# Kernel optimization log

Measured on AMD Instinct MI355X. Metric: run time of the kernel, lower is better.

## Reference

```python
import jax, jax.numpy as jnp
import numpy as np

G = 5   # grid intervals
K = 5   # spline order
H = 2.0 / G  # knot spacing on [-1, 1]
# Extended uniform knot vector: G + 2K + 1 = 16 knots from -1-K*H to 1+K*H.
KNOTS = jnp.arange(-K, G + K + 1, dtype=jnp.float32) * H - 1.0  # (16,)


def bspline_bases(x):
    """Cox-de Boor B-spline bases. x: (B, in) -> (B, in, G+K)."""
    g = KNOTS[None, :]            # (1, 16), broadcasts over (B, in, .)
    xe = x[..., None]             # (B, in, 1)
    # degree-0 indicator bases: (B, in, G+2K)
    b = ((xe >= g[:, :-1]) & (xe < g[:, 1:])).astype(x.dtype)
    for d in range(1, K + 1):
        left = (xe - g[:, : -(d + 1)]) / (g[:, d:-1] - g[:, : -(d + 1)]) * b[..., :-1]
        right = (g[:, d + 1 :] - xe) / (g[:, d + 1 :] - g[:, 1:-d]) * b[..., 1:]
        b = left + right
    return b  # (B, in, G+K)


def kan_layer(x, Wb, Ws):
    # residual base path: silu(x) @ Wb  (in,out)
    # spline path: sum_i sum_k B[b,i,k] * Ws[i,o,k]
    bases = bspline_bases(x)
    return jax.nn.silu(x) @ Wb + jnp.einsum('bik,iok->bo', bases, Ws)


def setup_inputs() -> dict:
    key = jax.random.key(0)
    ks = jax.random.split(key, 7)
    B, IN, OUT, NB = 16384, 1024, 64, G + K
    s = 0.1  # small init scale
    return {
        'x':   jax.random.uniform(ks[0], (B, IN), dtype=jnp.float32),
        'Wb1': jax.random.normal(ks[1], (IN, 5), dtype=jnp.float32) * s,
        'Ws1': jax.random.normal(ks[2], (IN, 5, NB), dtype=jnp.float32) * s,
        'Wb2': jax.random.normal(ks[3], (5, 5), dtype=jnp.float32) * s,
        'Ws2': jax.random.normal(ks[4], (5, 5, NB), dtype=jnp.float32) * s,
        'Wb3': jax.random.normal(ks[5], (5, OUT), dtype=jnp.float32) * s,
        'Ws3': jax.random.normal(ks[6], (5, OUT, NB), dtype=jnp.float32) * s,
    }


def reference(x, Wb1, Ws1, Wb2, Ws2, Wb3, Ws3):
    h = kan_layer(x, Wb1, Ws1)   # (B, 5)
    h = kan_layer(h, Wb2, Ws2)   # (B, 5)
    h = kan_layer(h, Wb3, Ws3)   # (B, 64)
    return jax.nn.softmax(h, axis=-1)
```

## Files before the change

kernel.cpp:

```cpp
#include <hip/hip_runtime.h>
#include <cstdint>
#include <cstddef>


#define NROWS 16384
#define IN1   1024

__global__ void k0_pack(const float* __restrict__ Wb1, const float* __restrict__ Ws1,
                        float* __restrict__ w4) {
  int e = blockIdx.x * 256 + threadIdx.x;
  int g = e >> 12, rem = e & 4095, i = rem >> 2, c = rem & 3;
  int slot = g * 4 + c;
  float v = 0.0f;
  if (slot < 40) {
    int o = slot >> 3, k = (slot & 7) + 2;
    v = Ws1[(i * 5 + o) * 10 + k];
  } else if (slot < 45) {
    v = Wb1[i * 5 + (slot - 40)];
  }
  w4[(size_t)g * 4096 + i * 4 + c] = v;
}

#define C120(a) ((a) / 120.0f)

__device__ __forceinline__ void kan1_bases(float x, float (&B)[8], float& si) {
  float v  = fmaf(x, 2.5f, 7.5f);
  float u  = __builtin_amdgcn_fractf(v);
  float N0 = fmaf(fmaf(fmaf(fmaf(fmaf(C120(-1.f), u, C120(5.f)),  u, C120(-10.f)), u, C120(10.f)),  u, C120(-5.f)),  u, C120(1.f));
  float N1 = fmaf(fmaf(fmaf(fmaf(fmaf(C120(5.f),  u, C120(-20.f)), u, C120(20.f)),  u, C120(20.f)),  u, C120(-50.f)), u, C120(26.f));
  float N2 = fmaf(fmaf(fmaf(fmaf(fmaf(C120(-10.f),u, C120(30.f)),  u, C120(0.f)),   u, C120(-60.f)), u, C120(0.f)),   u, C120(66.f));
  float N3 = fmaf(fmaf(fmaf(fmaf(fmaf(C120(10.f), u, C120(-20.f)), u, C120(-20.f)), u, C120(20.f)),  u, C120(50.f)),  u, C120(26.f));
  float N4 = fmaf(fmaf(fmaf(fmaf(fmaf(C120(-5.f), u, C120(5.f)),   u, C120(10.f)),  u, C120(10.f)),  u, C120(5.f)),   u, C120(1.f));
  float u2 = u * u;
  float N5 = u2 * u2 * u * C120(1.f);
  bool e0 = v < 8.0f;
  bool e2 = v >= 9.0f;
  B[0] = e0 ? N0 : 0.0f;
  B[1] = e0 ? N1 : (e2 ? 0.0f : N0);
  B[2] = e0 ? N2 : (e2 ? N0 : N1);
  B[3] = e0 ? N3 : (e2 ? N1 : N2);
  B[4] = e0 ? N4 : (e2 ? N2 : N3);
  B[5] = e0 ? N5 : (e2 ? N3 : N4);
  B[6] = e0 ? 0.0f : (e2 ? N4 : N5);
  B[7] = e2 ? N5 : 0.0f;
  si = x * __builtin_amdgcn_rcpf(1.0f + __expf(-x));
}

__device__ __forceinline__ void bases10(float xv, float* bb) {
  float v = fmaf(xv, 2.5f, 7.5f);
  float b[15];
#pragma unroll
  for (int j = 0; j < 15; ++j)
    b[j] = (v >= (float)j && v < (float)(j + 1)) ? 1.0f : 0.0f;
#pragma unroll
  for (int d = 1; d <= 5; ++d) {
    const float inv = 1.0f / (float)d;
#pragma unroll
    for (int j = 0; j + d < 15; ++j) {
      float left  = (v - (float)j) * inv;
      float right = ((float)(j + d + 1) - v) * inv;
      b[j] = left * b[j] + right * b[j + 1];
    }
  }
#pragma unroll
  for (int k = 0; k < 10; ++k) bb[k] = b[k];
}

__global__ __launch_bounds__(256, 4) void k1_fused(
    const float* __restrict__ x, const float* __restrict__ w4,
    const float* __restrict__ Wb2, const float* __restrict__ Ws2,
    const float* __restrict__ Wb3, const float* __restrict__ Ws3,
    float* __restrict__ out) {
  __shared__ float part[4][20];
  __shared__ float lsi1[16 * 5];
  __shared__ float lb1 [16 * 55];
  __shared__ float lsi2[16 * 5];
  __shared__ float lb2 [16 * 55];
  __shared__ float llog[16 * 65];
  __shared__ float lred[16 * 16];
  __shared__ float lmx [16];
  __shared__ float linv[16];

  int tid  = threadIdx.x;
  int wv   = tid >> 6, lane = tid & 63;
  int b    = blockIdx.x;
  int row0 = b * 16 + wv * 4;

  const float*  xb = x + (size_t)row0 * IN1 + lane;
  const float4* wp = (const float4*)w4 + lane;

  float acc[4][5];
#pragma unroll
  for (int r = 0; r < 4; ++r)
#pragma unroll
    for (int o = 0; o < 5; ++o) acc[r][o] = 0.0f;

#pragma unroll 1
  for (int s = 0; s < 16; ++s) {
    const float* xs = xb + s * 64;
    float B[4][8];
    float si[4];
    {
      float xv0 = xs[0];
      float xv1 = xs[IN1];
      float xv2 = xs[2 * IN1];
      float xv3 = xs[3 * IN1];
      kan1_bases(xv0, B[0], si[0]);
      kan1_bases(xv1, B[1], si[1]);
      kan1_bases(xv2, B[2], si[2]);
      kan1_bases(xv3, B[3], si[3]);
    }
    const float4* wps = wp + s * 64;
#pragma unroll
    for (int g = 0; g < 10; ++g) {
      float4 q = wps[(size_t)g * 1024];
      const int o0 = (4 * g) >> 3,     r0 = (4 * g) & 7;
      const int o1 = (4 * g + 1) >> 3, r1 = (4 * g + 1) & 7;
      const int o2 = (4 * g + 2) >> 3, r2 = (4 * g + 2) & 7;
      const int o3 = (4 * g + 3) >> 3, r3 = (4 * g + 3) & 7;
#pragma unroll
      for (int r = 0; r < 4; ++r) {
        acc[r][o0] = fmaf(B[r][r0], q.x, acc[r][o0]);
        acc[r][o1] = fmaf(B[r][r1], q.y, acc[r][o1]);
        acc[r][o2] = fmaf(B[r][r2], q.z, acc[r][o2]);
        acc[r][o3] = fmaf(B[r][r3], q.w, acc[r][o3]);
      }
    }
    {
      float4 q = wps[(size_t)10 * 1024];
#pragma unroll
      for (int r = 0; r < 4; ++r) {
        acc[r][0] = fmaf(si[r], q.x, acc[r][0]);
        acc[r][1] = fmaf(si[r], q.y, acc[r][1]);
        acc[r][2] = fmaf(si[r], q.z, acc[r][2]);
        acc[r][3] = fmaf(si[r], q.w, acc[r][3]);
      }
    }
    {
      float4 q = wps[(size_t)11 * 1024];
#pragma unroll
      for (int r = 0; r < 4; ++r)
        acc[r][4] = fmaf(si[r], q.x, acc[r][4]);
    }
  }

#pragma unroll
  for (int r = 0; r < 4; ++r)
#pragma unroll
    for (int o = 0; o < 5; ++o) {
      float v = acc[r][o];
#pragma unroll
      for (int m = 1; m < 64; m <<= 1) v += __shfl_xor(v, m);
      acc[r][o] = v;
    }
  if (lane == 0) {
#pragma unroll
    for (int r = 0; r < 4; ++r)
#pragma unroll
      for (int o = 0; o < 5; ++o) part[wv][r * 5 + o] = acc[r][o];
  }
  __syncthreads();

  if (tid < 80) {
    int row = tid & 15, i = tid >> 4;
    float s = part[row >> 2][(row & 3) * 5 + i];
    lsi1[row * 5 + i] = s / (1.0f + __expf(-s));
    float bb[10];
    bases10(s, bb);
#pragma unroll
    for (int k = 0; k < 10; ++k) lb1[row * 55 + i * 11 + k] = bb[k];
  }
  __syncthreads();

  if (tid < 80) {
    int row = tid & 15, o = tid >> 4;
    float a = 0.f;
#pragma unroll
    for (int i = 0; i < 5; ++i) {
      a = fmaf(lsi1[row * 5 + i], Wb2[i * 5 + o], a);
#pragma unroll
      for (int k = 0; k < 10; ++k)
        a = fmaf(lb1[row * 55 + i * 11 + k], Ws2[(i * 5 + o) * 10 + k], a);
    }
    lsi2[row * 5 + o] = a / (1.0f + __expf(-a));
    float bb[10];
    bases10(a, bb);
#pragma unroll
    for (int k = 0; k < 10; ++k) lb2[row * 55 + o * 11 + k] = bb[k];
  }
  __syncthreads();

  {
    int o  = tid & 63;
    int r0 = (tid >> 6) * 4;
    float lg[4] = {0.f, 0.f, 0.f, 0.f};
#pragma unroll
    for (int i = 0; i < 5; ++i) {
      float wbv = Wb3[i * 64 + o];
      float w[10];
#pragma unroll
      for (int k = 0; k < 10; ++k) w[k] = Ws3[(i * 64 + o) * 10 + k];
#pragma unroll
      for (int rr = 0; rr < 4; ++rr) {
        int row = r0 + rr;
        lg[rr] = fmaf(lsi2[row * 5 + i], wbv, lg[rr]);
#pragma unroll
        for (int k = 0; k < 10; ++k)
          lg[rr] = fmaf(lb2[row * 55 + i * 11 + k], w[k], lg[rr]);
      }
    }
#pragma unroll
    for (int rr = 0; rr < 4; ++rr) llog[(r0 + rr) * 65 + o] = lg[rr];
  }
  __syncthreads();

  int q = tid >> 4, row = tid & 15;
  {
    float m = -1e30f;
#pragma unroll
    for (int oo = 0; oo < 4; ++oo)
      m = fmaxf(m, llog[row * 65 + q * 4 + oo]);
    lred[q * 16 + row] = m;
  }
  __syncthreads();
  if (tid < 16) {
    float m = -1e30f;
#pragma unroll
    for (int k = 0; k < 16; ++k) m = fmaxf(m, lred[k * 16 + tid]);
    lmx[tid] = m;
  }
  __syncthreads();
  {
    float m = lmx[row];
    float s = 0.f;
#pragma unroll
    for (int oo = 0; oo < 4; ++oo) {
      int idx = row * 65 + q * 4 + oo;
      float e = __expf(llog[idx] - m);
      llog[idx] = e;
      s += e;
    }
    lred[q * 16 + row] = s;
  }
  __syncthreads();
  if (tid < 16) {
    float s = 0.f;
#pragma unroll
    for (int k = 0; k < 16; ++k) s += lred[k * 16 + tid];
    linv[tid] = 1.0f / s;
  }
  __syncthreads();
#pragma unroll
  for (int uu = 0; uu < 4; ++uu) {
    int u = tid + uu * 256;
    int r = u >> 6, o = u & 63;
    out[(size_t)(b * 16 + r) * 64 + o] = llog[r * 65 + o] * linv[r];
  }
}

extern "C" void kernel_launch(void* const* d_in, const int* in_sizes, int n_in,
                              void* d_out, int out_size, void* d_ws, size_t ws_size,
                              hipStream_t stream) {
  const float* x   = (const float*)d_in[0];
  const float* Wb1 = (const float*)d_in[1];
  const float* Ws1 = (const float*)d_in[2];
  const float* Wb2 = (const float*)d_in[3];
  const float* Ws2 = (const float*)d_in[4];
  const float* Wb3 = (const float*)d_in[5];
  const float* Ws3 = (const float*)d_in[6];
  float* out = (float*)d_out;

  float* w4 = (float*)d_ws;

  hipLaunchKernelGGL(k0_pack, dim3(192), dim3(256), 0, stream, Wb1, Ws1, w4);
  hipLaunchKernelGGL(k1_fused, dim3(NROWS / 16), dim3(256), 0, stream,
                     x, w4, Wb2, Ws2, Wb3, Ws3, out);
}
```

Measured before the change: 151.2 us.

## Halve rows per block, raise occupancy, and prefetch next x slice

Each block now handles 8 rows instead of 16 (2 per wave), and twice as many blocks are launched. Launch bounds go from 4 to 8 blocks per SM. The x values for the next 64-column slice are loaded one iteration ahead to hide global load latency. The aim is more waves in flight to cover memory latency on the 64 MB x stream. In exchange, the packed weights are reread twice as often per row and the tail stages use half the threads.

```diff
diff --git a/kernel.cpp b/kernel.cpp
--- a/kernel.cpp
+++ b/kernel.cpp
@@ -66,70 +66,69 @@
   for (int k = 0; k < 10; ++k) bb[k] = b[k];
 }
 
-__global__ __launch_bounds__(256, 4) void k1_fused(
+__global__ __launch_bounds__(256, 8) void k1_fused(
     const float* __restrict__ x, const float* __restrict__ w4,
     const float* __restrict__ Wb2, const float* __restrict__ Ws2,
     const float* __restrict__ Wb3, const float* __restrict__ Ws3,
     float* __restrict__ out) {
-  __shared__ float part[4][20];
-  __shared__ float lsi1[16 * 5];
-  __shared__ float lb1 [16 * 55];
-  __shared__ float lsi2[16 * 5];
-  __shared__ float lb2 [16 * 55];
-  __shared__ float llog[16 * 65];
-  __shared__ float lred[16 * 16];
-  __shared__ float lmx [16];
-  __shared__ float linv[16];
+  __shared__ float part[4][10];
+  __shared__ float lsi1[8 * 5];
+  __shared__ float lb1 [8 * 55];
+  __shared__ float lsi2[8 * 5];
+  __shared__ float lb2 [8 * 55];
+  __shared__ float llog[8 * 65];
+  __shared__ float lred[32 * 8];
+  __shared__ float lmx [8];
+  __shared__ float linv[8];
 
   int tid  = threadIdx.x;
   int wv   = tid >> 6, lane = tid & 63;
   int b    = blockIdx.x;
-  int row0 = b * 16 + wv * 4;
+  int row0 = b * 8 + wv * 2;
 
   const float*  xb = x + (size_t)row0 * IN1 + lane;
   const float4* wp = (const float4*)w4 + lane;
 
-  float acc[4][5];
-#pragma unroll
-  for (int r = 0; r < 4; ++r)
+  float acc[2][5];
+#pragma unroll
+  for (int r = 0; r < 2; ++r)
 #pragma unroll
     for (int o = 0; o < 5; ++o) acc[r][o] = 0.0f;
+
+  float xv0 = xb[0];
+  float xv1 = xb[IN1];
 
 #pragma unroll 1
   for (int s = 0; s < 16; ++s) {
-    const float* xs = xb + s * 64;
-    float B[4][8];
-    float si[4];
-    {
-      float xv0 = xs[0];
-      float xv1 = xs[IN1];
-      float xv2 = xs[2 * IN1];
-      float xv3 = xs[3 * IN1];
-      kan1_bases(xv0, B[0], si[0]);
-      kan1_bases(xv1, B[1], si[1]);
-      kan1_bases(xv2, B[2], si[2]);
-      kan1_bases(xv3, B[3], si[3]);
-    }
+    int sn = (s < 15) ? s + 1 : 15;
+    float xn0 = xb[(size_t)sn * 64];
+    float xn1 = xb[(size_t)sn * 64 + IN1];
+
+    float B[2][8];
+    float si[2];
+    kan1_bases(xv0, B[0], si[0]);
+    kan1_bases(xv1, B[1], si[1]);
+
     const float4* wps = wp + s * 64;
 #pragma unroll
     for (int g = 0; g < 10; ++g) {
       float4 q = wps[(size_t)g * 1024];
-      const int o0 = (4 * g) >> 3,     r0 = (4 * g) & 7;
-      const int o1 = (4 * g + 1) >> 3, r1 = (4 * g + 1) & 7;
-      const int o2 = (4 * g + 2) >> 3, r2 = (4 * g + 2) & 7;
-      const int o3 = (4 * g + 3) >> 3, r3 = (4 * g + 3) & 7;
-#pragma unroll
-      for (int r = 0; r < 4; ++r) {
-        acc[r][o0] = fmaf(B[r][r0], q.x, acc[r][o0]);
-        acc[r][o1] = fmaf(B[r][r1], q.y, acc[r][o1]);
-        acc[r][o2] = fmaf(B[r][r2], q.z, acc[r][o2]);
-        acc[r][o3] = fmaf(B[r][r3], q.w, acc[r][o3]);
+      const int o0 = (4 * g) >> 3,     k0 = (4 * g) & 7;
+      const int o1 = (4 * g + 1) >> 3, k1 = (4 * g + 1) & 7;
+      const int o2 = (4 * g + 2) >> 3, k2 = (4 * g + 2) & 7;
+      const int o3 = (4 * g + 3) >> 3, k3 = (4 * g + 3) & 7;
+#pragma unroll
+      for (int r = 0; r < 2; ++r) {
+        acc[r][o0] = fmaf(B[r][k0], q.x, acc[r][o0]);
+        acc[r][o1] = fmaf(B[r][k1], q.y, acc[r][o1]);
+        acc[r][o2] = fmaf(B[r][k2], q.z, acc[r][o2]);
+        acc[r][o3] = fmaf(B[r][k3], q.w, acc[r][o3]);
       }
     }
     {
       float4 q = wps[(size_t)10 * 1024];
 #pragma unroll
-      for (int r = 0; r < 4; ++r) {
+      for (int r = 0; r < 2; ++r) {
         acc[r][0] = fmaf(si[r], q.x, acc[r][0]);
         acc[r][1] = fmaf(si[r], q.y, acc[r][1]);
         acc[r][2] = fmaf(si[r], q.z, acc[r][2]);
@@ -139,13 +138,15 @@
     {
       float4 q = wps[(size_t)11 * 1024];
 #pragma unroll
-      for (int r = 0; r < 4; ++r)
+      for (int r = 0; r < 2; ++r)
         acc[r][4] = fmaf(si[r], q.x, acc[r][4]);
     }
-  }
-
-#pragma unroll
-  for (int r = 0; r < 4; ++r)
+    xv0 = xn0;
+    xv1 = xn1;
+  }
+
+#pragma unroll
+  for (int r = 0; r < 2; ++r)
 #pragma unroll
     for (int o = 0; o < 5; ++o) {
       float v = acc[r][o];
@@ -155,15 +156,15 @@
     }
   if (lane == 0) {
 #pragma unroll
-    for (int r = 0; r < 4; ++r)
+    for (int r = 0; r < 2; ++r)
 #pragma unroll
       for (int o = 0; o < 5; ++o) part[wv][r * 5 + o] = acc[r][o];
   }
   __syncthreads();
 
-  if (tid < 80) {
-    int row = tid & 15, i = tid >> 4;
-    float s = part[row >> 2][(row & 3) * 5 + i];
+  if (tid < 40) {
+    int row = tid & 7, i = tid >> 3;
+    float s = part[row >> 1][(row & 1) * 5 + i];
     lsi1[row * 5 + i] = s / (1.0f + __expf(-s));
     float bb[10];
     bases10(s, bb);
@@ -172,8 +173,8 @@
   }
   __syncthreads();
 
-  if (tid < 80) {
-    int row = tid & 15, o = tid >> 4;
+  if (tid < 40) {
+    int row = tid & 7, o = tid >> 3;
     float a = 0.f;
 #pragma unroll
     for (int i = 0; i < 5; ++i) {
@@ -192,8 +193,8 @@
 
   {
     int o  = tid & 63;
-    int r0 = (tid >> 6) * 4;
-    float lg[4] = {0.f, 0.f, 0.f, 0.f};
+    int r0 = (tid >> 6) * 2;
+    float lg[2] = {0.f, 0.f};
 #pragma unroll
     for (int i = 0; i < 5; ++i) {
       float wbv = Wb3[i * 64 + o];
@@ -201,7 +202,7 @@
 #pragma unroll
       for (int k = 0; k < 10; ++k) w[k] = Ws3[(i * 64 + o) * 10 + k];
 #pragma unroll
-      for (int rr = 0; rr < 4; ++rr) {
+      for (int rr = 0; rr < 2; ++rr) {
         int row = r0 + rr;
         lg[rr] = fmaf(lsi2[row * 5 + i], wbv, lg[rr]);
 #pragma unroll
@@ -210,23 +211,20 @@
       }
     }
 #pragma unroll
-    for (int rr = 0; rr < 4; ++rr) llog[(r0 + rr) * 65 + o] = lg[rr];
-  }
-  __syncthreads();
-
-  int q = tid >> 4, row = tid & 15;
+    for (int rr = 0; rr < 2; ++rr) llog[(r0 + rr) * 65 + o] = lg[rr];
+  }
+  __syncthreads();
+
+  int q = tid >> 3, row = tid & 7;
   {
+    float m = fmaxf(llog[row * 65 + q * 2], llog[row * 65 + q * 2 + 1]);
+    lred[q * 8 + row] = m;
+  }
+  __syncthreads();
+  if (tid < 8) {
     float m = -1e30f;
 #pragma unroll
-    for (int oo = 0; oo < 4; ++oo)
-      m = fmaxf(m, llog[row * 65 + q * 4 + oo]);
-    lred[q * 16 + row] = m;
-  }
-  __syncthreads();
-  if (tid < 16) {
-    float m = -1e30f;
-#pragma unroll
-    for (int k = 0; k < 16; ++k) m = fmaxf(m, lred[k * 16 + tid]);
+    for (int k = 0; k < 32; ++k) m = fmaxf(m, lred[k * 8 + tid]);
     lmx[tid] = m;
   }
   __syncthreads();
@@ -234,27 +232,27 @@
     float m = lmx[row];
     float s = 0.f;
 #pragma unroll
-    for (int oo = 0; oo < 4; ++oo) {
-      int idx = row * 65 + q * 4 + oo;
+    for (int oo = 0; oo < 2; ++oo) {
+      int idx = row * 65 + q * 2 + oo;
       float e = __expf(llog[idx] - m);
       llog[idx] = e;
       s += e;
     }
-    lred[q * 16 + row] = s;
-  }
-  __syncthreads();
-  if (tid < 16) {
+    lred[q * 8 + row] = s;
+  }
+  __syncthreads();
+  if (tid < 8) {
     float s = 0.f;
 #pragma unroll
-    for (int k = 0; k < 16; ++k) s += lred[k * 16 + tid];
+    for (int k = 0; k < 32; ++k) s += lred[k * 8 + tid];
     linv[tid] = 1.0f / s;
   }
   __syncthreads();
 #pragma unroll
-  for (int uu = 0; uu < 4; ++uu) {
+  for (int uu = 0; uu < 2; ++uu) {
     int u = tid + uu * 256;
     int r = u >> 6, o = u & 63;
-    out[(size_t)(b * 16 + r) * 64 + o] = llog[r * 65 + o] * linv[r];
+    out[(size_t)(b * 8 + r) * 64 + o] = llog[r * 65 + o] * linv[r];
   }
 }
 
@@ -273,6 +271,6 @@
   float* w4 = (float*)d_ws;
 
   hipLaunchKernelGGL(k0_pack, dim3(192), dim3(256), 0, stream, Wb1, Ws1, w4);
-  hipLaunchKernelGGL(k1_fused, dim3(NROWS / 16), dim3(256), 0, stream,
+  hipLaunchKernelGGL(k1_fused, dim3(NROWS / 8), dim3(256), 0, stream,
                      x, w4, Wb2, Ws2, Wb3, Ws3, out);
 }
```

Measured after the change: 183.8 us. +21.6%, slower.
